# Kernel optimization log

Measured on AMD Instinct MI355X. Metric: run time of the kernel, lower is better.

Reference implementation:

```python
import jax, jax.numpy as jnp
import numpy as np

B, N, D = 16, 1369, 1024
HID, NH = 512, 8
SCALE = np.sqrt(D // NH)


def _pos_encoding_2d(n, d):
    ps = int(np.sqrt(n))  # 37; n is a perfect square here
    div = jnp.exp(jnp.arange(0, d // 2, 2, dtype=jnp.float32) * (-np.log(10000.0) / (d // 2)))
    rows = (jnp.arange(n) // ps).astype(jnp.float32)
    cols = (jnp.arange(n) % ps).astype(jnp.float32)
    def interleave(s, c):
        return jnp.stack([s, c], axis=-1).reshape(n, -1)
    half_row = interleave(jnp.sin(rows[:, None] * div), jnp.cos(rows[:, None] * div))
    half_col = interleave(jnp.sin(cols[:, None] * div), jnp.cos(cols[:, None] * div))
    return jnp.concatenate([half_row, half_col], axis=-1)  # [n, d]


def _center_bias(n, strength=0.3):
    ps = int(np.sqrt(n))
    c = ps // 2
    y, x = jnp.meshgrid(jnp.arange(ps, dtype=jnp.float32), jnp.arange(ps, dtype=jnp.float32), indexing='ij')
    d2 = (x - c) ** 2 + (y - c) ** 2
    sigma = ps / 6.0
    return (jnp.exp(-d2 / (2.0 * sigma ** 2)).reshape(-1)) * strength  # [n]


def setup_inputs() -> dict:
    key = jax.random.key(0)
    ks = jax.random.split(key, 16)
    s = 0.02
    return {
        'patch_tokens': jax.random.normal(ks[0], (B, N, D), dtype=jnp.float32),
        'curiosity_score': jax.random.uniform(ks[1], (B,), dtype=jnp.float32),
        'Wq': jax.random.normal(ks[2], (D, D), dtype=jnp.float32) * s,
        'bq': jax.random.uniform(ks[3], (D,), minval=-0.05, maxval=0.05, dtype=jnp.float32),
        'Wk': jax.random.normal(ks[4], (D, D), dtype=jnp.float32) * s,
        'bk': jax.random.uniform(ks[5], (D,), minval=-0.05, maxval=0.05, dtype=jnp.float32),
        'Wv': jax.random.normal(ks[6], (D, D), dtype=jnp.float32) * s,
        'bv': jnp.zeros((D,), dtype=jnp.float32),
        'Wc1': jax.random.normal(ks[7], (1, HID // 8), dtype=jnp.float32) * s,
        'bc1': jnp.zeros((HID // 8,), dtype=jnp.float32),
        'Wc2': jax.random.normal(ks[8], (HID // 8, NH), dtype=jnp.float32) * s,
        'bc2': jnp.zeros((NH,), dtype=jnp.float32),
        'Wp1': jax.random.normal(ks[9], (D, HID), dtype=jnp.float32) * s,
        'bp1': jnp.zeros((HID,), dtype=jnp.float32),
        'Wp2': jax.random.normal(ks[10], (HID, HID // 4), dtype=jnp.float32) * s,
        'bp2': jnp.zeros((HID // 4,), dtype=jnp.float32),
        'adaptive_weight': jnp.float32(0.5),
    }


def reference(patch_tokens, curiosity_score, Wq, bq, Wk, bk, Wv, bv,
              Wc1, bc1, Wc2, bc2, Wp1, bp1, Wp2, bp2, adaptive_weight):
    b, n, d = patch_tokens.shape
    x = patch_tokens + _pos_encoding_2d(n, d)[None]  # [B,N,D]

    q = x @ Wq + bq
    k = x @ Wk + bk
    v = x @ Wv + bv

    scores = jnp.einsum('bqd,bkd->bqk', q, k) / SCALE          # [B,N,N]
    attn = jax.nn.softmax(scores, axis=-1)                     # dropout p=0 / eval
    attended = jnp.einsum('bqk,bkd->bqd', attn, v)             # [B,N,D]

    cb = _center_bias(n)[None]                                 # [1,N]
    VAR_EPS = 1e-6

    pa = attn.mean(axis=1) + cb
    # fallback chain (data-dependent in torch; expressed with jnp.where)
    pa2 = jnp.diagonal(attn, axis1=-2, axis2=-1) + cb
    pa = jnp.where(jnp.var(pa, ddof=1) < VAR_EPS, pa2, pa)
    pa3 = attn.max(axis=-1) + cb
    pa = jnp.where(jnp.var(pa, ddof=1) < VAR_EPS, pa3, pa)
    norms = jnp.linalg.norm(x, axis=-1)
    noise = jax.random.normal(jax.random.key(42), norms.shape, dtype=norms.dtype) * 0.1 * jnp.std(norms, ddof=1)
    pa = jnp.where(jnp.var(pa, ddof=1) < VAR_EPS, norms + noise, pa)

    pa = pa / (pa.sum(axis=-1, keepdims=True) + 1e-8)

    # curiosity modulation
    h = jax.nn.relu(curiosity_score[:, None] @ Wc1 + bc1)
    cm = jax.nn.sigmoid(h @ Wc2 + bc2)                         # [B,NH]
    cw = cm.mean(axis=-1, keepdims=True)                       # [B,1]
    modulated = pa * (1.0 + cw)
    fa = adaptive_weight * modulated + (1.0 - adaptive_weight) * pa

    fa = jnp.clip(fa, 1e-8, None)
    fa = fa / (fa.sum(axis=-1, keepdims=True) + 1e-8)

    weighted = jnp.sum(attended * fa[..., None], axis=1)       # [B,D]
    focal = jax.nn.relu(weighted @ Wp1 + bp1) @ Wp2 + bp2      # [B,HID//4]
    return focal, fa
```

## Files before the change

kernel.cpp:

```cpp
#include <hip/hip_runtime.h>
#include <hip/hip_bf16.h>
#include <cstdint>

#define B_   16
#define N_   1369
#define NP   1536
#define D_   1024
#define NQKV 3072
#define SLD  1568
#define QLD  3104

typedef __bf16 bf16x8_t __attribute__((ext_vector_type(8)));
typedef __bf16 bf16x4_t __attribute__((ext_vector_type(4)));
typedef float  f32x4_t  __attribute__((ext_vector_type(4)));

__device__ __forceinline__ float  bf2f(__bf16 x) { return (float)x; }
__device__ __forceinline__ __bf16 f2bf(float x)  { return (__bf16)x; }

#define GLOAD_LDS16(g, l) __builtin_amdgcn_global_load_lds( \
    (const __attribute__((address_space(1))) void*)(g),     \
    (__attribute__((address_space(3))) void*)(l), 16, 0, 0)

__global__ __launch_bounds__(256)
void pos_kernel(float* __restrict__ pos)
{
    const int idx = blockIdx.x * 256 + threadIdx.x;
    if (idx >= N_ * D_) return;
    const int n = idx >> 10, f = idx & 1023;
    const int row = n / 37, col = n - row * 37;
    const float base = (f < 512) ? (float)row : (float)col;
    const int  t2   = (f & 511) >> 1;
    const float dv  = __expf(-0.03597789207803197f * (float)t2);
    const float ang = base * dv;
    pos[idx] = (f & 1) ? cosf(ang) : sinf(ang);
}

__global__ __launch_bounds__(256)
void addpos_kernel(const float* __restrict__ patch, const float* __restrict__ pos,
                   __bf16* __restrict__ X)
{
    const long tid = (long)blockIdx.x * 256 + threadIdx.x;
    const long e   = tid * 4;
    const int  f   = (int)(e & 1023);
    const long nb  = e >> 10;
    const int  n   = (int)(nb % NP);
    const long b   = nb / NP;
    bf16x4_t o;
    if (n < N_) {
        const float4 p = *(const float4*)(patch + ((b * N_ + n) << 10) + f);
        const float4 q = *(const float4*)(pos + ((long)n << 10) + f);
        o[0] = f2bf(p.x + q.x); o[1] = f2bf(p.y + q.y);
        o[2] = f2bf(p.z + q.z); o[3] = f2bf(p.w + q.w);
    } else {
        o[0] = o[1] = o[2] = o[3] = f2bf(0.f);
    }
    *(bf16x4_t*)(X + e) = o;
}

__global__ __launch_bounds__(256)
void wcast_kernel(const float* __restrict__ W0, const float* __restrict__ W1,
                  const float* __restrict__ W2,
                  __bf16* __restrict__ T0, __bf16* __restrict__ T1, __bf16* __restrict__ T2)
{
    const float* W = blockIdx.z == 0 ? W0 : (blockIdx.z == 1 ? W1 : W2);
    __bf16*      T = blockIdx.z == 0 ? T0 : (blockIdx.z == 1 ? T1 : T2);
    __shared__ float tile[64][65];
    const int o0 = blockIdx.x * 64, i0 = blockIdx.y * 64;
    const int t = threadIdx.x;
    const int tr = t >> 4, tc = (t & 15) * 4;
    #pragma unroll
    for (int rr = 0; rr < 64; rr += 16) {
        float4 v = *(const float4*)(W + (long)(i0 + rr + tr) * 1024 + o0 + tc);
        tile[rr + tr][tc + 0] = v.x; tile[rr + tr][tc + 1] = v.y;
        tile[rr + tr][tc + 2] = v.z; tile[rr + tr][tc + 3] = v.w;
    }
    __syncthreads();
    #pragma unroll
    for (int rr = 0; rr < 64; rr += 16) {
        bf16x4_t o;
        o[0] = f2bf(tile[tc + 0][rr + tr]); o[1] = f2bf(tile[tc + 1][rr + tr]);
        o[2] = f2bf(tile[tc + 2][rr + tr]); o[3] = f2bf(tile[tc + 3][rr + tr]);
        *(bf16x4_t*)(T + (long)(o0 + rr + tr) * 1024 + i0 + tc) = o;
    }
}

__global__ __launch_bounds__(256)
void bcat_kernel(const float* __restrict__ bq, const float* __restrict__ bk,
                 const float* __restrict__ bv, float* __restrict__ bcat)
{
    const int i = blockIdx.x * 256 + threadIdx.x;
    if (i >= NQKV) return;
    const int p = i >> 10, j = i & 1023;
    bcat[i] = p == 0 ? bq[j] : (p == 1 ? bk[j] : bv[j]);
}

template<int HAS_BIAS, int STATS>
__global__ __launch_bounds__(1024, 4)
void gemm256(const __bf16* __restrict__ A, const __bf16* __restrict__ Bt,
             __bf16* __restrict__ C, const float* __restrict__ bias,
             float2* __restrict__ mzp,
             int lda, int ldb, int ldc, int Kd, float scale,
             long sA, long sB, long sC, int tilesN, int tilesPerBatch, int cpx)
{
    __shared__ __bf16 lds[65536];
    const int bid = blockIdx.x;
    const int vt  = (bid & 7) * cpx + (bid >> 3);
    const int bz  = vt / tilesPerBatch;
    const int rem = vt - bz * tilesPerBatch;
    const int ty  = rem / tilesN;
    const int tx  = rem - ty * tilesN;
    A  += (long)bz * sA;  Bt += (long)bz * sB;  C += (long)bz * sC;
    const int m0 = ty * 256, n0 = tx * 256;

    const int t  = threadIdx.x;
    const int w  = t >> 6, l = t & 63;
    const int wr = w >> 2, wc = w & 3;
    const int lr = l & 15, lh = l >> 4;

    const int laneF  = (lr * 64 + ((lh * 16) ^ (((lr >> 3) & 1) << 5))) >> 1;
    const int rstage = (w >> 1) * 16 + (l >> 2);
    const int kstage = (w & 1) * 32 + (((l & 3) * 8) ^ (((l >> 5) & 1) << 4));

    const __bf16* Ag = A  + (long)(m0 + rstage) * lda + kstage;
    const __bf16* Bg = Bt + (long)(n0 + rstage) * ldb + kstage;
    __bf16* dA = lds + w * 512;
    __bf16* dB = lds + 16384 + w * 512;

#define SA_(buf, half, kt) GLOAD_LDS16(Ag + (long)(half) * 128 * lda + (kt) * 64, \
                                       dA + (buf) * 32768 + (half) * 8192)
#define SB_(buf, half, kt) GLOAD_LDS16(Bg + (long)(half) * 128 * ldb + (kt) * 64, \
                                       dB + (buf) * 32768 + (half) * 8192)

    f32x4_t acc[4][4] = {};

    const int NT = Kd >> 6;
    SA_(0, 0, 0); SA_(0, 1, 0); SB_(0, 0, 0); SB_(0, 1, 0);
    asm volatile("s_waitcnt vmcnt(0)" ::: "memory");
    __builtin_amdgcn_s_barrier();

    for (int tk = 0; tk < NT; ++tk) {
        const int c = tk & 1, o = c ^ 1;
        if (tk + 1 < NT) {
            SA_(o, 0, tk + 1); SA_(o, 1, tk + 1);
            SB_(o, 0, tk + 1); SB_(o, 1, tk + 1);
        }
        const int cb = c * 32768;
        const __bf16* ap = lds + cb + (wr >> 1) * 8192 + (wr & 1) * 4096 + laneF;
        const __bf16* bp = lds + cb + 16384 + (wc >> 1) * 8192 + (wc & 1) * 4096 + laneF;
        bf16x8_t af[4], bfm[4];
        #pragma unroll
        for (int nn = 0; nn < 4; ++nn) bfm[nn] = *(const bf16x8_t*)(bp + nn * 1024);
        #pragma unroll
        for (int mi = 0; mi < 4; ++mi) af[mi]  = *(const bf16x8_t*)(ap + mi * 1024);
        __builtin_amdgcn_s_setprio(1);
        #pragma unroll
        for (int mi = 0; mi < 4; ++mi)
            #pragma unroll
            for (int nn = 0; nn < 4; ++nn)
                acc[mi][nn] = __builtin_amdgcn_mfma_f32_16x16x32_bf16(af[mi], bfm[nn], acc[mi][nn], 0, 0, 0);
        __builtin_amdgcn_s_setprio(0);
        #pragma unroll
        for (int nn = 0; nn < 4; ++nn) bfm[nn] = *(const bf16x8_t*)(bp + nn * 1024 + 512);
        #pragma unroll
        for (int mi = 0; mi < 4; ++mi) af[mi]  = *(const bf16x8_t*)(ap + mi * 1024 + 512);
        __builtin_amdgcn_s_setprio(1);
        #pragma unroll
        for (int mi = 0; mi < 4; ++mi)
            #pragma unroll
            for (int nn = 0; nn < 4; ++nn)
                acc[mi][nn] = __builtin_amdgcn_mfma_f32_16x16x32_bf16(af[mi], bfm[nn], acc[mi][nn], 0, 0, 0);
        __builtin_amdgcn_s_setprio(0);
        asm volatile("s_waitcnt vmcnt(0)" ::: "memory");
        __builtin_amdgcn_s_barrier();
    }

    #pragma unroll
    for (int mi = 0; mi < 4; ++mi) {
        const int row = m0 + wr * 64 + mi * 16 + lh * 4;
        #pragma unroll
        for (int nn = 0; nn < 4; ++nn) {
            const int col = n0 + wc * 64 + nn * 16 + lr;
            const float bb = HAS_BIAS ? bias[col] : 0.0f;
            #pragma unroll
            for (int q = 0; q < 4; ++q)
                C[(long)(row + q) * ldc + col] = f2bf(acc[mi][nn][q] * scale + bb);
        }
    }

    if (STATS) {
        __syncthreads();
        float* lm = (float*)lds;
        float* lz = lm + 1024;
        #pragma unroll
        for (int mi = 0; mi < 4; ++mi) {
            #pragma unroll
            for (int qq = 0; qq < 4; ++qq) {
                float vb[4]; float m = -3.0e38f;
                #pragma unroll
                for (int nn = 0; nn < 4; ++nn) {
                    const int col = n0 + wc * 64 + nn * 16 + lr;
                    const float vr = bf2f(f2bf(acc[mi][nn][qq] * scale));
                    vb[nn] = (col < N_) ? vr : -3.0e38f;
                    m = fmaxf(m, vb[nn]);
                }
                #pragma unroll
                for (int o = 1; o <= 8; o <<= 1) m = fmaxf(m, __shfl_xor(m, o));
                float z = 0.f;
                #pragma unroll
                for (int nn = 0; nn < 4; ++nn) z += __expf(vb[nn] - m);
                #pragma unroll
                for (int o = 1; o <= 8; o <<= 1) z += __shfl_xor(z, o);
                if (lr == 0) {
                    const int r = wr * 64 + mi * 16 + lh * 4 + qq;
                    lm[r * 4 + wc] = m; lz[r * 4 + wc] = z;
                }
            }
        }
        __syncthreads();
        if (t < 256) {
            const float ma = lm[t * 4 + 0], mb = lm[t * 4 + 1];
            const float mc = lm[t * 4 + 2], md = lm[t * 4 + 3];
            const float M = fmaxf(fmaxf(ma, mb), fmaxf(mc, md));
            const float Z = lz[t * 4 + 0] * __expf(ma - M) + lz[t * 4 + 1] * __expf(mb - M)
                          + lz[t * 4 + 2] * __expf(mc - M) + lz[t * 4 + 3] * __expf(md - M);
            mzp[((long)bz * NP + ty * 256 + t) * 6 + tx] = make_float2(M, Z);
        }
    }
#undef SA_
#undef SB_
}

__global__ __launch_bounds__(256)
void combine_kernel(const float2* __restrict__ mzp,
                    float* __restrict__ rowM, float* __restrict__ rowZi)
{
    const int i = blockIdx.x * 256 + threadIdx.x;
    if (i >= B_ * NP) return;
    float2 p[6]; float M = -3.0e38f;
    #pragma unroll
    for (int k = 0; k < 6; ++k) { p[k] = mzp[(long)i * 6 + k]; M = fmaxf(M, p[k].x); }
    float Z = 0.f;
    #pragma unroll
    for (int k = 0; k < 6; ++k) Z += p[k].y * __expf(p[k].x - M);
    rowM[i]  = M;
    rowZi[i] = 1.f / Z;
}

template<int WEIGHTED>
__global__ __launch_bounds__(256)
void colsum_kernel(const __bf16* __restrict__ attn,
                   const float* __restrict__ rowM, const float* __restrict__ rowZi,
                   const float* __restrict__ wv, float* __restrict__ out)
{
    const int t = threadIdx.x;
    if (t >= 192) return;
    const int b  = blockIdx.y;
    const int q0 = blockIdx.x * 16;
    const int q1 = (q0 + 16 < N_) ? q0 + 16 : N_;
    const int k8 = t * 8;
    float s[8] = {};
    const __bf16* base = attn + (long)b * NP * SLD + k8;
    for (int q = q0; q < q1; ++q) {
        bf16x8_t v = *(const bf16x8_t*)(base + (long)q * SLD);
        const float Mq = rowM[b * NP + q];
        float wq = rowZi[b * NP + q];
        if (WEIGHTED) wq *= wv[b * NP + q];
        #pragma unroll
        for (int i = 0; i < 8; ++i) s[i] += wq * __expf(bf2f(v[i]) - Mq);
    }
    #pragma unroll
    for (int i = 0; i < 8; ++i) atomicAdd(out + b * NP + k8 + i, s[i]);
}

__global__ __launch_bounds__(256)
void fa_kernel(const float* __restrict__ pa_raw, const float* __restrict__ curiosity,
               const float* __restrict__ Wc1, const float* __restrict__ bc1,
               const float* __restrict__ Wc2, const float* __restrict__ bc2,
               const float* __restrict__ aw_p,
               float* __restrict__ fa_ws, float* __restrict__ out_fa)
{
    const int b = blockIdx.x, t = threadIdx.x;
    __shared__ float hsh[64];
    __shared__ float red[8];
    __shared__ float cwsh;
    if (t < 64) hsh[t] = fmaxf(0.f, curiosity[b] * Wc1[t] + bc1[t]);
    __syncthreads();
    if (t < 8) {
        float a = bc2[t];
        for (int j = 0; j < 64; ++j) a += hsh[j] * Wc2[j * 8 + t];
        red[t] = 1.f / (1.f + __expf(-a));
    }
    __syncthreads();
    if (t == 0) {
        float cw = 0.f;
        for (int i = 0; i < 8; ++i) cw += red[i];
        cwsh = cw * 0.125f;
    }
    __syncthreads();
    const float aw   = aw_p[0];
    const float modf = 1.f + aw * cwsh;
    const float sig  = 37.f / 6.f;
    const float inv2s2 = 1.f / (2.f * sig * sig);
    float pv[6];
    float s1 = 0.f;
    #pragma unroll
    for (int i = 0; i < 6; ++i) {
        const int k = t + i * 256;
        float p = 0.f;
        if (k < N_) {
            const int y = k / 37, x = k - y * 37;
            const float d2 = (float)((x - 18) * (x - 18) + (y - 18) * (y - 18));
            const float cb = 0.3f * __expf(-d2 * inv2s2);
            p = pa_raw[b * NP + k] * (1.f / 1369.f) + cb;
        }
        pv[i] = p; s1 += p;
    }
    #pragma unroll
    for (int o = 32; o; o >>= 1) s1 += __shfl_xor(s1, o);
    __syncthreads();
    if (!(t & 63)) red[t >> 6] = s1;
    __syncthreads();
    s1 = red[0] + red[1] + red[2] + red[3];
    const float inv1 = 1.f / (s1 + 1e-8f);
    float s2 = 0.f;
    #pragma unroll
    for (int i = 0; i < 6; ++i) {
        const int k = t + i * 256;
        if (k < N_) {
            const float f = fmaxf(pv[i] * inv1 * modf, 1e-8f);
            pv[i] = f; s2 += f;
        }
    }
    #pragma unroll
    for (int o = 32; o; o >>= 1) s2 += __shfl_xor(s2, o);
    if (!(t & 63)) red[4 + (t >> 6)] = s2;
    __syncthreads();
    s2 = red[4] + red[5] + red[6] + red[7];
    const float inv2 = 1.f / (s2 + 1e-8f);
    #pragma unroll
    for (int i = 0; i < 6; ++i) {
        const int k = t + i * 256;
        if (k < N_) {
            const float f = pv[i] * inv2;
            fa_ws[b * NP + k]  = f;
            out_fa[b * N_ + k] = f;
        }
    }
}

__global__ __launch_bounds__(256)
void weighted_kernel(const float* __restrict__ g, const __bf16* __restrict__ V,
                     int ldv, float* __restrict__ wout)
{
    const int b  = blockIdx.y;
    const int k0 = blockIdx.x * 86;
    const int k1 = (k0 + 86 < N_) ? k0 + 86 : N_;
    const int d  = threadIdx.x * 4;
    float a0 = 0, a1 = 0, a2 = 0, a3 = 0;
    const __bf16* vb = V + (long)b * NP * ldv + d;
    for (int k = k0; k < k1; ++k) {
        const float gv = g[b * NP + k];
        bf16x4_t vv = *(const bf16x4_t*)(vb + (long)k * ldv);
        a0 += gv * bf2f(vv[0]); a1 += gv * bf2f(vv[1]);
        a2 += gv * bf2f(vv[2]); a3 += gv * bf2f(vv[3]);
    }
    atomicAdd(wout + b * D_ + d + 0, a0);
    atomicAdd(wout + b * D_ + d + 1, a1);
    atomicAdd(wout + b * D_ + d + 2, a2);
    atomicAdd(wout + b * D_ + d + 3, a3);
}

__global__ __launch_bounds__(256)
void focal1_kernel(const float* __restrict__ weighted, const float* __restrict__ Wp1,
                   const float* __restrict__ bp1, float* __restrict__ h)
{
    const int b = blockIdx.y, jc = blockIdx.x;
    const int t = threadIdx.x;
    const int jl = t >> 2, part = t & 3;
    const int j = jc * 64 + jl;
    const float* wb = weighted + b * 1024 + part * 256;
    const float* wp = Wp1 + (long)(part * 256) * 512 + j;
    float a = 0.f;
    #pragma unroll 8
    for (int d = 0; d < 256; ++d) a += wb[d] * wp[(long)d * 512];
    a += __shfl_xor(a, 1);
    a += __shfl_xor(a, 2);
    if (part == 0) h[b * 512 + j] = fmaxf(a + bp1[j], 0.f);
}

__global__ __launch_bounds__(128)
void focal2_kernel(const float* __restrict__ h, const float* __restrict__ Wp2,
                   const float* __restrict__ bp2, float* __restrict__ out)
{
    const int b = blockIdx.x, o = threadIdx.x;
    __shared__ float hs[512];
    for (int i = o; i < 512; i += 128) hs[i] = h[b * 512 + i];
    __syncthreads();
    float a = bp2[o];
    #pragma unroll 8
    for (int j = 0; j < 512; ++j) a += hs[j] * Wp2[j * 128 + o];
    out[b * 128 + o] = a;
}

extern "C" void kernel_launch(void* const* d_in, const int* in_sizes, int n_in,
                              void* d_out, int out_size, void* d_ws, size_t ws_size,
                              hipStream_t stream)
{
    const float* patch     = (const float*)d_in[0];
    const float* curiosity = (const float*)d_in[1];
    const float* Wq  = (const float*)d_in[2];
    const float* bq  = (const float*)d_in[3];
    const float* Wk  = (const float*)d_in[4];
    const float* bk  = (const float*)d_in[5];
    const float* Wv  = (const float*)d_in[6];
    const float* bv  = (const float*)d_in[7];
    const float* Wc1 = (const float*)d_in[8];
    const float* bc1 = (const float*)d_in[9];
    const float* Wc2 = (const float*)d_in[10];
    const float* bc2 = (const float*)d_in[11];
    const float* Wp1 = (const float*)d_in[12];
    const float* bp1 = (const float*)d_in[13];
    const float* Wp2 = (const float*)d_in[14];
    const float* bp2 = (const float*)d_in[15];
    const float* aw  = (const float*)d_in[16];
    float* out = (float*)d_out;

    char* ws = (char*)d_ws;
    size_t off = 0;
    auto alloc = [&](size_t bytes) -> char* {
        char* p = ws + off;
        off += (bytes + 255) & ~(size_t)255;
        return p;
    };
    float*  pos  = (float*) alloc((size_t)N_ * D_ * 4);
    __bf16* X    = (__bf16*)alloc((size_t)B_ * NP * D_ * 2);
    __bf16* WT   = (__bf16*)alloc((size_t)3 * D_ * D_ * 2);
    const size_t S_BYTES = (size_t)B_ * NP * SLD * 2;
    if (off < S_BYTES) off = S_BYTES;
    __bf16* S    = (__bf16*)ws;
    __bf16* QKV  = (__bf16*)alloc((size_t)B_ * NP * QLD * 2);
    float*  pa   = (float*) alloc((size_t)B_ * NP * 4);
    float*  faw  = (float*) alloc((size_t)B_ * NP * 4);
    float*  gbuf = (float*) alloc((size_t)B_ * NP * 4);
    float*  wsum = (float*) alloc((size_t)B_ * D_ * 4);
    float*  bcat = (float*) alloc((size_t)NQKV * 4);
    float*  hbuf = (float*) alloc((size_t)B_ * 512 * 4);
    float2* mzp  = (float2*)alloc((size_t)B_ * NP * 6 * 8);
    float*  rowM = (float*) alloc((size_t)B_ * NP * 4);
    float*  rowZi= (float*) alloc((size_t)B_ * NP * 4);

    (void)hipMemsetAsync(pa,   0, (size_t)B_ * NP * 4, stream);
    (void)hipMemsetAsync(gbuf, 0, (size_t)B_ * NP * 4, stream);
    (void)hipMemsetAsync(wsum, 0, (size_t)B_ * D_ * 4, stream);

    pos_kernel<<<(N_ * D_ + 255) / 256, 256, 0, stream>>>(pos);
    addpos_kernel<<<(int)((size_t)B_ * NP * D_ / 4 / 256), 256, 0, stream>>>(patch, pos, X);
    {
        dim3 g(16, 16, 3);
        wcast_kernel<<<g, 256, 0, stream>>>(Wq, Wk, Wv,
                                            WT, WT + D_ * D_, WT + 2 * D_ * D_);
    }
    bcat_kernel<<<(NQKV + 255) / 256, 256, 0, stream>>>(bq, bk, bv, bcat);
    {
        const int nwg = 96 * 12;
        gemm256<1, 0><<<nwg, 1024, 0, stream>>>(X, WT, QKV, bcat, nullptr,
                                                D_, D_, QLD, D_, 1.0f,
                                                0, 0, 0, 12, nwg, nwg / 8);
    }
    {
        const int nwg = 36 * B_;
        gemm256<0, 1><<<nwg, 1024, 0, stream>>>(QKV, QKV + D_, S, nullptr, mzp,
                                                QLD, QLD, SLD, D_,
                                                0.08838834764831845f,
                                                (long)NP * QLD, (long)NP * QLD,
                                                (long)NP * SLD, 6, 36, nwg / 8);
    }
    combine_kernel<<<(B_ * NP + 255) / 256, 256, 0, stream>>>(mzp, rowM, rowZi);
    {
        dim3 g(86, B_);
        colsum_kernel<0><<<g, 256, 0, stream>>>(S, rowM, rowZi, nullptr, pa);
    }
    fa_kernel<<<B_, 256, 0, stream>>>(pa, curiosity, Wc1, bc1, Wc2, bc2, aw,
                                      faw, out + B_ * 128);
    {
        dim3 g(86, B_);
        colsum_kernel<1><<<g, 256, 0, stream>>>(S, rowM, rowZi, faw, gbuf);
    }
    {
        dim3 g(16, B_);
        weighted_kernel<<<g, 256, 0, stream>>>(gbuf, QKV + 2 * D_, QLD, wsum);
    }
    {
        dim3 g(8, B_);
        focal1_kernel<<<g, 256, 0, stream>>>(wsum, Wp1, bp1, hbuf);
    }
    focal2_kernel<<<B_, 128, 0, stream>>>(hbuf, Wp2, bp2, out);
}
```

Baseline: 552.7 us.

## Drop V projection by reassociating weighted sum through Wv; fuse combine into colsum

Instead of computing V = X·Wv for every token and then taking a weighted sum over tokens, the code first reduces X with the attention weights into a per-batch vector u and the weight sum, then applies Wv and bv once through a small GEMV. This cuts the QKV GEMM from three projections to two, shrinking its work and output buffer. The softmax combine kernel is folded into colsum, the memsets are merged into one, and score-GEMM stores are masked to valid rows and columns. The weighted sum now uses the bf16 X rather than bf16 V, which changes rounding slightly.

```diff
diff --git a/kernel.cpp b/kernel.cpp
--- a/kernel.cpp
+++ b/kernel.cpp
@@ -6,9 +6,9 @@
 #define N_   1369
 #define NP   1536
 #define D_   1024
-#define NQKV 3072
+#define NQK  2048
 #define SLD  1568
-#define QLD  3104
+#define QLD  2080
 
 typedef __bf16 bf16x8_t __attribute__((ext_vector_type(8)));
 typedef __bf16 bf16x4_t __attribute__((ext_vector_type(4)));
@@ -59,11 +59,10 @@
 
 __global__ __launch_bounds__(256)
 void wcast_kernel(const float* __restrict__ W0, const float* __restrict__ W1,
-                  const float* __restrict__ W2,
-                  __bf16* __restrict__ T0, __bf16* __restrict__ T1, __bf16* __restrict__ T2)
-{
-    const float* W = blockIdx.z == 0 ? W0 : (blockIdx.z == 1 ? W1 : W2);
-    __bf16*      T = blockIdx.z == 0 ? T0 : (blockIdx.z == 1 ? T1 : T2);
+                  __bf16* __restrict__ T0, __bf16* __restrict__ T1)
+{
+    const float* W = blockIdx.z == 0 ? W0 : W1;
+    __bf16*      T = blockIdx.z == 0 ? T0 : T1;
     __shared__ float tile[64][65];
     const int o0 = blockIdx.x * 64, i0 = blockIdx.y * 64;
     const int t = threadIdx.x;
@@ -86,21 +85,20 @@
 
 __global__ __launch_bounds__(256)
 void bcat_kernel(const float* __restrict__ bq, const float* __restrict__ bk,
-                 const float* __restrict__ bv, float* __restrict__ bcat)
+                 float* __restrict__ bcat)
 {
     const int i = blockIdx.x * 256 + threadIdx.x;
-    if (i >= NQKV) return;
-    const int p = i >> 10, j = i & 1023;
-    bcat[i] = p == 0 ? bq[j] : (p == 1 ? bk[j] : bv[j]);
+    if (i >= NQK) return;
+    bcat[i] = (i < 1024) ? bq[i] : bk[i - 1024];
 }
 
 template<int HAS_BIAS, int STATS>
-__global__ __launch_bounds__(1024, 4)
-void gemm256(const __bf16* __restrict__ A, const __bf16* __restrict__ Bt,
-             __bf16* __restrict__ C, const float* __restrict__ bias,
-             float2* __restrict__ mzp,
-             int lda, int ldb, int ldc, int Kd, float scale,
-             long sA, long sB, long sC, int tilesN, int tilesPerBatch, int cpx)
+__device__ __forceinline__
+void gemm_body(const __bf16* __restrict__ A, const __bf16* __restrict__ Bt,
+               __bf16* __restrict__ C, const float* __restrict__ bias,
+               float2* __restrict__ mzp,
+               int lda, int ldb, int ldc, int Kd, float scale,
+               long sA, long sB, long sC, int tilesN, int tilesPerBatch, int cpx)
 {
     __shared__ __bf16 lds[65536];
     const int bid = blockIdx.x;
@@ -182,8 +180,10 @@
             const int col = n0 + wc * 64 + nn * 16 + lr;
             const float bb = HAS_BIAS ? bias[col] : 0.0f;
             #pragma unroll
-            for (int q = 0; q < 4; ++q)
-                C[(long)(row + q) * ldc + col] = f2bf(acc[mi][nn][q] * scale + bb);
+            for (int q = 0; q < 4; ++q) {
+                if (!STATS || ((row + q) < N_ && col < N_))
+                    C[(long)(row + q) * ldc + col] = f2bf(acc[mi][nn][q] * scale + bb);
+            }
         }
     }
 
@@ -230,46 +230,64 @@
 #undef SB_
 }
 
-__global__ __launch_bounds__(256)
-void combine_kernel(const float2* __restrict__ mzp,
-                    float* __restrict__ rowM, float* __restrict__ rowZi)
-{
-    const int i = blockIdx.x * 256 + threadIdx.x;
-    if (i >= B_ * NP) return;
-    float2 p[6]; float M = -3.0e38f;
-    #pragma unroll
-    for (int k = 0; k < 6; ++k) { p[k] = mzp[(long)i * 6 + k]; M = fmaxf(M, p[k].x); }
-    float Z = 0.f;
-    #pragma unroll
-    for (int k = 0; k < 6; ++k) Z += p[k].y * __expf(p[k].x - M);
-    rowM[i]  = M;
-    rowZi[i] = 1.f / Z;
+__global__ __launch_bounds__(1024, 4)
+void gemm_qk(const __bf16* A, const __bf16* Bt, __bf16* C, const float* bias,
+             int lda, int ldb, int ldc, int Kd,
+             int tilesN, int tilesPerBatch, int cpx)
+{
+    gemm_body<1, 0>(A, Bt, C, bias, nullptr, lda, ldb, ldc, Kd, 1.0f,
+                    0, 0, 0, tilesN, tilesPerBatch, cpx);
+}
+
+__global__ __launch_bounds__(1024, 4)
+void gemm_sc(const __bf16* A, const __bf16* Bt, __bf16* C, float2* mzp,
+             int lda, int ldb, int ldc, int Kd, float scale,
+             long sA, long sB, long sC, int tilesN, int tilesPerBatch, int cpx)
+{
+    gemm_body<0, 1>(A, Bt, C, nullptr, mzp, lda, ldb, ldc, Kd, scale,
+                    sA, sB, sC, tilesN, tilesPerBatch, cpx);
 }
 
 template<int WEIGHTED>
 __global__ __launch_bounds__(256)
-void colsum_kernel(const __bf16* __restrict__ attn,
-                   const float* __restrict__ rowM, const float* __restrict__ rowZi,
+void colsum_kernel(const __bf16* __restrict__ attn, const float2* __restrict__ mzp,
                    const float* __restrict__ wv, float* __restrict__ out)
 {
-    const int t = threadIdx.x;
-    if (t >= 192) return;
+    const int t  = threadIdx.x;
     const int b  = blockIdx.y;
     const int q0 = blockIdx.x * 16;
-    const int q1 = (q0 + 16 < N_) ? q0 + 16 : N_;
+    __shared__ float sM[16], sZi[16];
+    if (t < 16) {
+        const int q = q0 + t;
+        float M = -3.0e38f, Zi = 1.f;
+        if (q < N_) {
+            float2 p[6];
+            #pragma unroll
+            for (int k = 0; k < 6; ++k) { p[k] = mzp[((long)b * NP + q) * 6 + k]; M = fmaxf(M, p[k].x); }
+            float Z = 0.f;
+            #pragma unroll
+            for (int k = 0; k < 6; ++k) Z += p[k].y * __expf(p[k].x - M);
+            Zi = 1.f / Z;
+        }
+        sM[t] = M; sZi[t] = Zi;
+    }
+    __syncthreads();
     const int k8 = t * 8;
-    float s[8] = {};
-    const __bf16* base = attn + (long)b * NP * SLD + k8;
-    for (int q = q0; q < q1; ++q) {
-        bf16x8_t v = *(const bf16x8_t*)(base + (long)q * SLD);
-        const float Mq = rowM[b * NP + q];
-        float wq = rowZi[b * NP + q];
-        if (WEIGHTED) wq *= wv[b * NP + q];
-        #pragma unroll
-        for (int i = 0; i < 8; ++i) s[i] += wq * __expf(bf2f(v[i]) - Mq);
-    }
-    #pragma unroll
-    for (int i = 0; i < 8; ++i) atomicAdd(out + b * NP + k8 + i, s[i]);
+    if (k8 < N_) {
+        const int q1 = (q0 + 16 < N_) ? q0 + 16 : N_;
+        float s[8] = {};
+        const __bf16* base = attn + (long)b * NP * SLD + k8;
+        for (int q = q0; q < q1; ++q) {
+            bf16x8_t v = *(const bf16x8_t*)(base + (long)q * SLD);
+            const float Mq = sM[q - q0];
+            float wq = sZi[q - q0];
+            if (WEIGHTED) wq *= wv[b * NP + q];
+            #pragma unroll
+            for (int i = 0; i < 8; ++i) s[i] += wq * __expf(bf2f(v[i]) - Mq);
+        }
+        #pragma unroll
+        for (int i = 0; i < 8; ++i) atomicAdd(out + b * NP + k8 + i, s[i]);
+    }
 }
 
 __global__ __launch_bounds__(256)
@@ -349,25 +367,45 @@
 }
 
 __global__ __launch_bounds__(256)
-void weighted_kernel(const float* __restrict__ g, const __bf16* __restrict__ V,
-                     int ldv, float* __restrict__ wout)
+void u_kernel(const float* __restrict__ g, const __bf16* __restrict__ X,
+              float* __restrict__ u, float* __restrict__ gsum)
 {
     const int b  = blockIdx.y;
     const int k0 = blockIdx.x * 86;
     const int k1 = (k0 + 86 < N_) ? k0 + 86 : N_;
     const int d  = threadIdx.x * 4;
-    float a0 = 0, a1 = 0, a2 = 0, a3 = 0;
-    const __bf16* vb = V + (long)b * NP * ldv + d;
+    float a0 = 0, a1 = 0, a2 = 0, a3 = 0, gs = 0;
+    const __bf16* xb = X + (long)b * NP * D_ + d;
     for (int k = k0; k < k1; ++k) {
         const float gv = g[b * NP + k];
-        bf16x4_t vv = *(const bf16x4_t*)(vb + (long)k * ldv);
-        a0 += gv * bf2f(vv[0]); a1 += gv * bf2f(vv[1]);
-        a2 += gv * bf2f(vv[2]); a3 += gv * bf2f(vv[3]);
-    }
-    atomicAdd(wout + b * D_ + d + 0, a0);
-    atomicAdd(wout + b * D_ + d + 1, a1);
-    atomicAdd(wout + b * D_ + d + 2, a2);
-    atomicAdd(wout + b * D_ + d + 3, a3);
+        bf16x4_t xv = *(const bf16x4_t*)(xb + (long)k * D_);
+        a0 += gv * bf2f(xv[0]); a1 += gv * bf2f(xv[1]);
+        a2 += gv * bf2f(xv[2]); a3 += gv * bf2f(xv[3]);
+        gs += gv;
+    }
+    atomicAdd(u + b * D_ + d + 0, a0);
+    atomicAdd(u + b * D_ + d + 1, a1);
+    atomicAdd(u + b * D_ + d + 2, a2);
+    atomicAdd(u + b * D_ + d + 3, a3);
+    if (threadIdx.x == 0) atomicAdd(gsum + b, gs);
+}
+
+__global__ __launch_bounds__(256)
+void wv_gemv_kernel(const float* __restrict__ u, const float* __restrict__ gsum,
+                    const float* __restrict__ Wv, const float* __restrict__ bv,
+                    float* __restrict__ wout)
+{
+    const int dcx = blockIdx.x, b = blockIdx.y;
+    const int t = threadIdx.x;
+    __shared__ float us[1024];
+    #pragma unroll
+    for (int i = 0; i < 4; ++i) us[t + i * 256] = u[b * D_ + t + i * 256];
+    __syncthreads();
+    const int d = dcx * 256 + t;
+    float a = gsum[b] * bv[d];
+    #pragma unroll 8
+    for (int i = 0; i < 1024; ++i) a += us[i] * Wv[(long)i * 1024 + d];
+    wout[b * D_ + d] = a;
 }
 
 __global__ __launch_bounds__(256)
@@ -434,61 +472,59 @@
     };
     float*  pos  = (float*) alloc((size_t)N_ * D_ * 4);
     __bf16* X    = (__bf16*)alloc((size_t)B_ * NP * D_ * 2);
-    __bf16* WT   = (__bf16*)alloc((size_t)3 * D_ * D_ * 2);
-    const size_t S_BYTES = (size_t)B_ * NP * SLD * 2;
-    if (off < S_BYTES) off = S_BYTES;
-    __bf16* S    = (__bf16*)ws;
-    __bf16* QKV  = (__bf16*)alloc((size_t)B_ * NP * QLD * 2);
+    __bf16* WT   = (__bf16*)alloc((size_t)2 * D_ * D_ * 2);
+    __bf16* S    = (__bf16*)alloc((size_t)B_ * NP * SLD * 2);
+    __bf16* QK   = (__bf16*)alloc((size_t)B_ * NP * QLD * 2);
     float*  pa   = (float*) alloc((size_t)B_ * NP * 4);
+    float*  gbuf = (float*) alloc((size_t)B_ * NP * 4);
+    float*  ubuf = (float*) alloc((size_t)B_ * D_ * 4);
+    float*  gsum = (float*) alloc((size_t)B_ * 4);
+    const size_t zbytes = (size_t)((char*)(gsum + B_) - (char*)pa);
     float*  faw  = (float*) alloc((size_t)B_ * NP * 4);
-    float*  gbuf = (float*) alloc((size_t)B_ * NP * 4);
-    float*  wsum = (float*) alloc((size_t)B_ * D_ * 4);
-    float*  bcat = (float*) alloc((size_t)NQKV * 4);
+    float*  bcat = (float*) alloc((size_t)NQK * 4);
     float*  hbuf = (float*) alloc((size_t)B_ * 512 * 4);
     float2* mzp  = (float2*)alloc((size_t)B_ * NP * 6 * 8);
-    float*  rowM = (float*) alloc((size_t)B_ * NP * 4);
-    float*  rowZi= (float*) alloc((size_t)B_ * NP * 4);
-
-    (void)hipMemsetAsync(pa,   0, (size_t)B_ * NP * 4, stream);
-    (void)hipMemsetAsync(gbuf, 0, (size_t)B_ * NP * 4, stream);
-    (void)hipMemsetAsync(wsum, 0, (size_t)B_ * D_ * 4, stream);
+    float*  wsum = (float*) alloc((size_t)B_ * D_ * 4);
+
+    (void)hipMemsetAsync(pa, 0, zbytes, stream);
 
     pos_kernel<<<(N_ * D_ + 255) / 256, 256, 0, stream>>>(pos);
     addpos_kernel<<<(int)((size_t)B_ * NP * D_ / 4 / 256), 256, 0, stream>>>(patch, pos, X);
     {
-        dim3 g(16, 16, 3);
-        wcast_kernel<<<g, 256, 0, stream>>>(Wq, Wk, Wv,
-                                            WT, WT + D_ * D_, WT + 2 * D_ * D_);
-    }
-    bcat_kernel<<<(NQKV + 255) / 256, 256, 0, stream>>>(bq, bk, bv, bcat);
-    {
-        const int nwg = 96 * 12;
-        gemm256<1, 0><<<nwg, 1024, 0, stream>>>(X, WT, QKV, bcat, nullptr,
-                                                D_, D_, QLD, D_, 1.0f,
-                                                0, 0, 0, 12, nwg, nwg / 8);
+        dim3 g(16, 16, 2);
+        wcast_kernel<<<g, 256, 0, stream>>>(Wq, Wk, WT, WT + D_ * D_);
+    }
+    bcat_kernel<<<(NQK + 255) / 256, 256, 0, stream>>>(bq, bk, bcat);
+    {
+        const int nwg = 96 * 8;
+        gemm_qk<<<nwg, 1024, 0, stream>>>(X, WT, QK, bcat,
+                                          D_, D_, QLD, D_, 8, nwg, nwg / 8);
     }
     {
         const int nwg = 36 * B_;
-        gemm256<0, 1><<<nwg, 1024, 0, stream>>>(QKV, QKV + D_, S, nullptr, mzp,
-                                                QLD, QLD, SLD, D_,
-                                                0.08838834764831845f,
-                                                (long)NP * QLD, (long)NP * QLD,
-                                                (long)NP * SLD, 6, 36, nwg / 8);
-    }
-    combine_kernel<<<(B_ * NP + 255) / 256, 256, 0, stream>>>(mzp, rowM, rowZi);
+        gemm_sc<<<nwg, 1024, 0, stream>>>(QK, QK + 1024, S, mzp,
+                                          QLD, QLD, SLD, D_,
+                                          0.08838834764831845f,
+                                          (long)NP * QLD, (long)NP * QLD,
+                                          (long)NP * SLD, 6, 36, nwg / 8);
+    }
     {
         dim3 g(86, B_);
-        colsum_kernel<0><<<g, 256, 0, stream>>>(S, rowM, rowZi, nullptr, pa);
+        colsum_kernel<0><<<g, 256, 0, stream>>>(S, mzp, nullptr, pa);
     }
     fa_kernel<<<B_, 256, 0, stream>>>(pa, curiosity, Wc1, bc1, Wc2, bc2, aw,
                                       faw, out + B_ * 128);
     {
         dim3 g(86, B_);
-        colsum_kernel<1><<<g, 256, 0, stream>>>(S, rowM, rowZi, faw, gbuf);
+        colsum_kernel<1><<<g, 256, 0, stream>>>(S, mzp, faw, gbuf);
     }
     {
         dim3 g(16, B_);
-        weighted_kernel<<<g, 256, 0, stream>>>(gbuf, QKV + 2 * D_, QLD, wsum);
+        u_kernel<<<g, 256, 0, stream>>>(gbuf, X, ubuf, gsum);
+    }
+    {
+        dim3 g(4, B_);
+        wv_gemv_kernel<<<g, 256, 0, stream>>>(ubuf, gsum, Wv, bv, wsum);
     }
     {
         dim3 g(8, B_);
```

After: 551.3 us. About the same (-0.3%).
